# Kernel optimization log

Measured on AMD Instinct MI355X. Metric: run time of the kernel, lower is better.

Reference implementation:

```python
import jax, jax.numpy as jnp
import numpy as np

N = 100_000      # nodes
E = 3_200_000    # edges (avg degree 32)
D_IN = 128
D_H = 128
EPS = 1e-12      # F.normalize eps


def setup_inputs() -> dict:
    key = jax.random.key(0)
    k1, k2, k3 = jax.random.split(key, 3)
    X = jax.random.normal(k1, (N, D_IN), dtype=jnp.float32)
    edge_index = jax.random.randint(k2, (2, E), 0, N, dtype=jnp.int32)
    # GCNConv linear weight (stored as [in, out] for X @ W) and bias
    W = jax.random.normal(k3, (D_IN, D_H), dtype=jnp.float32) / np.sqrt(D_IN)
    b = jnp.zeros((D_H,), dtype=jnp.float32)
    # MessageNorm learnable scale, init 1.0
    scale = jnp.ones((1,), dtype=jnp.float32)
    return {"X": X, "edge_index": edge_index, "W": W, "b": b, "scale": scale}


def reference(X, edge_index, W, b, scale):
    n = X.shape[0]
    loop = jnp.arange(n, dtype=edge_index.dtype)
    src = jnp.concatenate([edge_index[0], loop])  # add self loops
    tgt = jnp.concatenate([edge_index[1], loop])
    # symmetric GCN normalization: D^{-1/2} (A+I) D^{-1/2}
    deg = jax.ops.segment_sum(jnp.ones_like(src, X.dtype), tgt, num_segments=n)
    dinv = jnp.where(deg > 0, jax.lax.rsqrt(deg), 0.0)
    norm = dinv[src] * dinv[tgt]  # [E+N]
    XW = X @ W  # [N, D_H]
    msg = jax.ops.segment_sum(norm[:, None] * XW[src], tgt, num_segments=n) + b
    # MessageNorm(learn_scale=True): l2-normalize msg, rescale by ||x||_2 * scale
    msg_n = msg / jnp.maximum(jnp.linalg.norm(msg, axis=-1, keepdims=True), EPS)
    x_norm = jnp.linalg.norm(X, axis=-1, keepdims=True)
    return jax.nn.gelu(msg_n * x_norm * scale, approximate=False)
```

## Files before the change

kernel.cpp:

```cpp
#include <hip/hip_runtime.h>
#include <math.h>

#define D 128
#define NB 391
#define BSH 8
#define BMASK 255
#define CAP 10240
#define EPB 4096
#define LDA 136

typedef unsigned short ushort_t;
typedef unsigned int uint_t;
typedef __attribute__((ext_vector_type(8))) short bfrag;
typedef __attribute__((ext_vector_type(4))) float ffrag;

__device__ inline ushort_t f2bf(float f) {
    uint_t u = __float_as_uint(f);
    uint_t r = (u + 0x7FFFu + ((u >> 16) & 1u)) >> 16;
    return (ushort_t)r;
}

__global__ __launch_bounds__(256) void k_bin(const int* __restrict__ src,
                                             const int* __restrict__ tgt, int e,
                                             int* __restrict__ bucket_cur,
                                             uint_t* __restrict__ binned,
                                             const float* __restrict__ W,
                                             ushort_t* __restrict__ Wt) {
    __shared__ int lcnt[NB];
    __shared__ int lbase[NB];
    int tid = threadIdx.x;

    if (blockIdx.x < 16) {
        int nrow = blockIdx.x * 8 + (tid >> 5);
        int k0 = (tid & 31) * 4;
        ushort4 o;
        o.x = f2bf(W[(size_t)(k0 + 0) * D + nrow]);
        o.y = f2bf(W[(size_t)(k0 + 1) * D + nrow]);
        o.z = f2bf(W[(size_t)(k0 + 2) * D + nrow]);
        o.w = f2bf(W[(size_t)(k0 + 3) * D + nrow]);
        *(ushort4*)&Wt[(size_t)nrow * D + k0] = o;
    }

    int base = blockIdx.x * EPB;
    for (int i = tid; i < NB; i += 256) lcnt[i] = 0;
    __syncthreads();

    int myb[16], myrank[16];
    uint_t myval[16];
#pragma unroll
    for (int k = 0; k < 16; ++k) {
        int i = base + k * 256 + tid;
        if (i < e) {
            int t = tgt[i];
            int s = src[i];
            int b = t >> BSH;
            myb[k] = b;
            myval[k] = ((uint_t)s << BSH) | (uint_t)(t & BMASK);
            myrank[k] = atomicAdd(&lcnt[b], 1);
        } else {
            myb[k] = -1;
        }
    }
    __syncthreads();
    for (int i = tid; i < NB; i += 256) {
        int c = lcnt[i];
        lbase[i] = (c > 0) ? atomicAdd(&bucket_cur[i], c) : 0;
    }
    __syncthreads();
#pragma unroll
    for (int k = 0; k < 16; ++k) {
        if (myb[k] >= 0) {
            int slot = lbase[myb[k]] + myrank[k];
            if (slot < CAP) binned[(size_t)myb[k] * CAP + slot] = myval[k];
        }
    }
}

__global__ __launch_bounds__(256) void k_sort(const uint_t* __restrict__ binned,
                                              const int* __restrict__ bucket_cur,
                                              int* __restrict__ col,
                                              int* __restrict__ rowptr,
                                              float* __restrict__ dinv, int n) {
    __shared__ uint_t sout[CAP];
    __shared__ int scnt[256];
    __shared__ int sincl[256];
    __shared__ int sofs[256];
    __shared__ int sred[256];
    int b = blockIdx.x;
    int tid = threadIdx.x;

    int v = 0;
    for (int i = tid; i < b; i += 256) v += min(bucket_cur[i], CAP);
    sred[tid] = v;
    __syncthreads();
    for (int off = 128; off >= 1; off >>= 1) {
        if (tid < off) sred[tid] += sred[tid + off];
        __syncthreads();
    }
    int baseg = sred[0];

    int nb = min(bucket_cur[b], CAP);
    const uint_t* bin = binned + (size_t)b * CAP;

    scnt[tid] = 0;
    __syncthreads();
    for (int i = tid; i < nb; i += 256)
        atomicAdd(&scnt[bin[i] & BMASK], 1);
    __syncthreads();
    int x = scnt[tid];
    sincl[tid] = x;
    __syncthreads();
    for (int off = 1; off < 256; off <<= 1) {
        int y = (tid >= off) ? sincl[tid - off] : 0;
        __syncthreads();
        x += y;
        sincl[tid] = x;
        __syncthreads();
    }
    sofs[tid] = x - scnt[tid];
    int t = (b << BSH) + tid;
    if (t < n) {
        rowptr[t + 1] = baseg + x;
        dinv[t] = rsqrtf((float)scnt[tid] + 1.0f);
    }
    if (b == 0 && tid == 0) rowptr[0] = 0;
    __syncthreads();
    for (int i = tid; i < nb; i += 256) {
        uint_t w = bin[i];
        int r = atomicAdd(&sofs[w & BMASK], 1);
        sout[r] = w >> BSH;
    }
    __syncthreads();
    for (int i = tid; i < nb; i += 256)
        col[baseg + i] = (int)sout[i];
}

__global__ __launch_bounds__(256) void k_gemm(const float* __restrict__ X,
                                              const ushort_t* __restrict__ Wt,
                                              const float* __restrict__ dinv,
                                              ushort_t* __restrict__ Y,
                                              float* __restrict__ xnorm, int n) {
    __shared__ ushort_t As[64 * LDA];
    __shared__ ushort_t Bs[128 * LDA];
    int tid = threadIdx.x;
    int row0 = blockIdx.x * 64;

    for (int i = tid; i < 128 * 16; i += 256) {
        int nr = i >> 4, c = (i & 15) << 3;
        *(uint4*)&Bs[nr * LDA + c] = *(const uint4*)&Wt[(size_t)nr * D + c];
    }

    const float4* X4 = (const float4*)X;
#pragma unroll
    for (int i2 = 0; i2 < 8; ++i2) {
        int item = i2 * 256 + tid;
        int r = item >> 5, c4 = item & 31;
        int gr = row0 + r;
        float4 v = (gr < n) ? X4[(size_t)gr * 32 + c4] : make_float4(0.f, 0.f, 0.f, 0.f);
        ushort4 bv;
        bv.x = f2bf(v.x); bv.y = f2bf(v.y); bv.z = f2bf(v.z); bv.w = f2bf(v.w);
        *(ushort4*)&As[r * LDA + c4 * 4] = bv;
        float s = v.x * v.x + v.y * v.y + v.z * v.z + v.w * v.w;
        s += __shfl_xor(s, 1);
        s += __shfl_xor(s, 2);
        s += __shfl_xor(s, 4);
        s += __shfl_xor(s, 8);
        s += __shfl_xor(s, 16);
        if ((tid & 31) == 0 && gr < n) xnorm[gr] = sqrtf(s);
    }
    __syncthreads();

    int w = tid >> 6;
    int lane = tid & 63;
    int q = lane >> 4;
    int mi = lane & 15;

    bfrag xf[4];
#pragma unroll
    for (int kt = 0; kt < 4; ++kt)
        xf[kt] = *(const bfrag*)&As[(w * 16 + mi) * LDA + kt * 32 + q * 8];

    ffrag acc[8];
#pragma unroll
    for (int nt = 0; nt < 8; ++nt) acc[nt] = (ffrag){0.f, 0.f, 0.f, 0.f};

#pragma unroll
    for (int nt = 0; nt < 8; ++nt) {
#pragma unroll
        for (int kt = 0; kt < 4; ++kt) {
            bfrag wf = *(const bfrag*)&Bs[(nt * 16 + mi) * LDA + kt * 32 + q * 8];
            acc[nt] = __builtin_amdgcn_mfma_f32_16x16x32_bf16(wf, xf[kt], acc[nt], 0, 0, 0);
        }
    }

    int gr = row0 + w * 16 + mi;
    if (gr < n) {
        float dv = dinv[gr];
#pragma unroll
        for (int nt = 0; nt < 8; ++nt) {
            ushort4 o;
            o.x = f2bf(acc[nt][0] * dv);
            o.y = f2bf(acc[nt][1] * dv);
            o.z = f2bf(acc[nt][2] * dv);
            o.w = f2bf(acc[nt][3] * dv);
            *(ushort4*)&Y[(size_t)gr * D + nt * 16 + q * 4] = o;
        }
    }
}

__global__ __launch_bounds__(256) void k_agg(const ushort_t* __restrict__ Y,
                                             const float* __restrict__ xnorm,
                                             const float* __restrict__ dinv,
                                             const int* __restrict__ rowptr,
                                             const int* __restrict__ col,
                                             const float* __restrict__ bias,
                                             const float* __restrict__ scale,
                                             float* __restrict__ out, int n) {
    int t = (blockIdx.x * 256 + threadIdx.x) >> 6;
    int lane = threadIdx.x & 63;
    if (t >= n) return;

    const char* Yb = (const char*)Y;
    uint_t lo4 = (uint_t)lane * 4;

    uint_t p = *(const uint_t*)(Yb + (((uint_t)t << 8) + lo4));
    float a0 = __uint_as_float(p << 16);
    float a1 = __uint_as_float(p & 0xFFFF0000u);

    int beg = rowptr[t];
    int end = rowptr[t + 1];
    for (int base = beg; base < end; base += 64) {
        int m = min(end - base, 64);
        uint_t cv = (uint_t)col[base + min(lane, m - 1)];
        int k = 0;
        for (; k + 16 <= m; k += 16) {
            uint_t qv[16];
#pragma unroll
            for (int j = 0; j < 16; ++j) {
                uint_t s = (uint_t)__builtin_amdgcn_readlane((int)cv, k + j);
                qv[j] = *(const uint_t*)(Yb + ((size_t)s << 8) + lo4);
            }
#pragma unroll
            for (int j = 0; j < 16; ++j) {
                a0 += __uint_as_float(qv[j] << 16);
                a1 += __uint_as_float(qv[j] & 0xFFFF0000u);
            }
        }
        for (; k + 4 <= m; k += 4) {
            uint_t qv[4];
#pragma unroll
            for (int j = 0; j < 4; ++j) {
                uint_t s = (uint_t)__builtin_amdgcn_readlane((int)cv, k + j);
                qv[j] = *(const uint_t*)(Yb + ((size_t)s << 8) + lo4);
            }
#pragma unroll
            for (int j = 0; j < 4; ++j) {
                a0 += __uint_as_float(qv[j] << 16);
                a1 += __uint_as_float(qv[j] & 0xFFFF0000u);
            }
        }
        for (; k < m; ++k) {
            uint_t s = (uint_t)__builtin_amdgcn_readlane((int)cv, k);
            uint_t q = *(const uint_t*)(Yb + ((size_t)s << 8) + lo4);
            a0 += __uint_as_float(q << 16);
            a1 += __uint_as_float(q & 0xFFFF0000u);
        }
    }

    float dt = dinv[t];
    float m0 = fmaf(dt, a0, bias[lane * 2]);
    float m1 = fmaf(dt, a1, bias[lane * 2 + 1]);

    float m2 = m0 * m0 + m1 * m1;
#pragma unroll
    for (int m = 32; m >= 1; m >>= 1) m2 += __shfl_xor(m2, m);

    float denom = fmaxf(sqrtf(m2), 1e-12f);
    float fac = xnorm[t] * scale[0] / denom;
    float g0 = m0 * fac;
    float g1 = m1 * fac;
    float2 o;
    o.x = 0.5f * g0 * (1.0f + erff(g0 * 0.70710678118654752440f));
    o.y = 0.5f * g1 * (1.0f + erff(g1 * 0.70710678118654752440f));
    *(float2*)&out[(size_t)t * D + lane * 2] = o;
}


extern "C" void kernel_launch(void* const* d_in, const int* in_sizes, int n_in,
                              void* d_out, int out_size, void* d_ws, size_t ws_size,
                              hipStream_t stream) {
    const float* X     = (const float*)d_in[0];
    const int*   ei    = (const int*)d_in[1];
    const float* W     = (const float*)d_in[2];
    const float* bias  = (const float*)d_in[3];
    const float* scale = (const float*)d_in[4];
    float* out = (float*)d_out;

    int n = in_sizes[0] / D;
    int e = in_sizes[1] / 2;
    const int* src = ei;
    const int* tgt = ei + e;

    char* ws = (char*)d_ws;
    ushort_t* Y = (ushort_t*)ws;   ws += (size_t)n * D * sizeof(ushort_t);
    uint_t* binned = (uint_t*)Y;
    float* dinv = (float*)ws;      ws += (size_t)n * sizeof(float);
    float* xnorm = (float*)ws;     ws += (size_t)n * sizeof(float);
    int* rowptr = (int*)ws;        ws += (size_t)(n + 1) * sizeof(int);
    int* bucket_cur = (int*)ws;    ws += NB * sizeof(int);
    int* col = (int*)ws;           ws += (size_t)e * sizeof(int);
    ushort_t* Wt = (ushort_t*)ws;

    hipMemsetAsync(bucket_cur, 0, NB * sizeof(int), stream);
    k_bin<<<(e + EPB - 1) / EPB, 256, 0, stream>>>(src, tgt, e, bucket_cur, binned, W, Wt);
    k_sort<<<NB, 256, 0, stream>>>(binned, bucket_cur, col, rowptr, dinv, n);
    k_gemm<<<(n + 63) / 64, 256, 0, stream>>>(X, Wt, dinv, Y, xnorm, n);
    k_agg<<<(n + 3) / 4, 256, 0, stream>>>(Y, xnorm, dinv, rowptr, col, bias, scale, out, n);
}
```

Baseline: 308.0 us.

## Fuse per-bucket CSR sort into aggregation kernel and drop separate sort pass

Removes the k_sort kernel. Edges are binned into smaller 64-target buckets, and each aggregation block sorts its own bucket's sources in shared memory before gathering, so the col/rowptr arrays are never written to or read back from global memory. Degrees are now counted with a global atomic per edge in k_bin, and the GEMM computes dinv inline from them. The cost is 3.2M global atomics on deg, and bins get a separate workspace region instead of aliasing Y. There is also overflow risk: CAP=2432 per 64-node bucket, while the expected load is about 2048.

```diff
diff --git a/kernel.cpp b/kernel.cpp
--- a/kernel.cpp
+++ b/kernel.cpp
@@ -2,11 +2,12 @@
 #include <math.h>
 
 #define D 128
-#define NB 391
-#define BSH 8
-#define BMASK 255
-#define CAP 10240
-#define EPB 4096
+#define BSH 6
+#define BMASK 63
+#define NT 64
+#define NB 1563
+#define CAP 2432
+#define EPB 8192
 #define LDA 136
 
 typedef unsigned short ushort_t;
@@ -20,17 +21,18 @@
     return (ushort_t)r;
 }
 
-__global__ __launch_bounds__(256) void k_bin(const int* __restrict__ src,
+__global__ __launch_bounds__(512) void k_bin(const int* __restrict__ src,
                                              const int* __restrict__ tgt, int e,
                                              int* __restrict__ bucket_cur,
                                              uint_t* __restrict__ binned,
+                                             int* __restrict__ deg,
                                              const float* __restrict__ W,
                                              ushort_t* __restrict__ Wt) {
     __shared__ int lcnt[NB];
     __shared__ int lbase[NB];
     int tid = threadIdx.x;
 
-    if (blockIdx.x < 16) {
+    if (blockIdx.x < 16 && tid < 256) {
         int nrow = blockIdx.x * 8 + (tid >> 5);
         int k0 = (tid & 31) * 4;
         ushort4 o;
@@ -42,14 +44,14 @@
     }
 
     int base = blockIdx.x * EPB;
-    for (int i = tid; i < NB; i += 256) lcnt[i] = 0;
+    for (int i = tid; i < NB; i += 512) lcnt[i] = 0;
     __syncthreads();
 
     int myb[16], myrank[16];
     uint_t myval[16];
 #pragma unroll
     for (int k = 0; k < 16; ++k) {
-        int i = base + k * 256 + tid;
+        int i = base + k * 512 + tid;
         if (i < e) {
             int t = tgt[i];
             int s = src[i];
@@ -57,12 +59,13 @@
             myb[k] = b;
             myval[k] = ((uint_t)s << BSH) | (uint_t)(t & BMASK);
             myrank[k] = atomicAdd(&lcnt[b], 1);
+            atomicAdd(&deg[t], 1);
         } else {
             myb[k] = -1;
         }
     }
     __syncthreads();
-    for (int i = tid; i < NB; i += 256) {
+    for (int i = tid; i < NB; i += 512) {
         int c = lcnt[i];
         lbase[i] = (c > 0) ? atomicAdd(&bucket_cur[i], c) : 0;
     }
@@ -76,68 +79,9 @@
     }
 }
 
-__global__ __launch_bounds__(256) void k_sort(const uint_t* __restrict__ binned,
-                                              const int* __restrict__ bucket_cur,
-                                              int* __restrict__ col,
-                                              int* __restrict__ rowptr,
-                                              float* __restrict__ dinv, int n) {
-    __shared__ uint_t sout[CAP];
-    __shared__ int scnt[256];
-    __shared__ int sincl[256];
-    __shared__ int sofs[256];
-    __shared__ int sred[256];
-    int b = blockIdx.x;
-    int tid = threadIdx.x;
-
-    int v = 0;
-    for (int i = tid; i < b; i += 256) v += min(bucket_cur[i], CAP);
-    sred[tid] = v;
-    __syncthreads();
-    for (int off = 128; off >= 1; off >>= 1) {
-        if (tid < off) sred[tid] += sred[tid + off];
-        __syncthreads();
-    }
-    int baseg = sred[0];
-
-    int nb = min(bucket_cur[b], CAP);
-    const uint_t* bin = binned + (size_t)b * CAP;
-
-    scnt[tid] = 0;
-    __syncthreads();
-    for (int i = tid; i < nb; i += 256)
-        atomicAdd(&scnt[bin[i] & BMASK], 1);
-    __syncthreads();
-    int x = scnt[tid];
-    sincl[tid] = x;
-    __syncthreads();
-    for (int off = 1; off < 256; off <<= 1) {
-        int y = (tid >= off) ? sincl[tid - off] : 0;
-        __syncthreads();
-        x += y;
-        sincl[tid] = x;
-        __syncthreads();
-    }
-    sofs[tid] = x - scnt[tid];
-    int t = (b << BSH) + tid;
-    if (t < n) {
-        rowptr[t + 1] = baseg + x;
-        dinv[t] = rsqrtf((float)scnt[tid] + 1.0f);
-    }
-    if (b == 0 && tid == 0) rowptr[0] = 0;
-    __syncthreads();
-    for (int i = tid; i < nb; i += 256) {
-        uint_t w = bin[i];
-        int r = atomicAdd(&sofs[w & BMASK], 1);
-        sout[r] = w >> BSH;
-    }
-    __syncthreads();
-    for (int i = tid; i < nb; i += 256)
-        col[baseg + i] = (int)sout[i];
-}
-
 __global__ __launch_bounds__(256) void k_gemm(const float* __restrict__ X,
                                               const ushort_t* __restrict__ Wt,
-                                              const float* __restrict__ dinv,
+                                              const int* __restrict__ deg,
                                               ushort_t* __restrict__ Y,
                                               float* __restrict__ xnorm, int n) {
     __shared__ ushort_t As[64 * LDA];
@@ -195,7 +139,7 @@
 
     int gr = row0 + w * 16 + mi;
     if (gr < n) {
-        float dv = dinv[gr];
+        float dv = rsqrtf((float)deg[gr] + 1.0f);
 #pragma unroll
         for (int nt = 0; nt < 8; ++nt) {
             ushort4 o;
@@ -210,79 +154,119 @@
 
 __global__ __launch_bounds__(256) void k_agg(const ushort_t* __restrict__ Y,
                                              const float* __restrict__ xnorm,
-                                             const float* __restrict__ dinv,
-                                             const int* __restrict__ rowptr,
-                                             const int* __restrict__ col,
+                                             const uint_t* __restrict__ binned,
+                                             const int* __restrict__ bucket_cur,
                                              const float* __restrict__ bias,
                                              const float* __restrict__ scale,
                                              float* __restrict__ out, int n) {
-    int t = (blockIdx.x * 256 + threadIdx.x) >> 6;
-    int lane = threadIdx.x & 63;
-    if (t >= n) return;
+    __shared__ uint_t ssrc[CAP];
+    __shared__ int scnt[NT];
+    __shared__ int sbeg[NT];
+    __shared__ int sofs[NT];
+    int b = blockIdx.x;
+    int tid = threadIdx.x;
+    int wv = tid >> 6;
+    int lane = tid & 63;
+
+    int nb = min(bucket_cur[b], CAP);
+    const uint_t* bin = binned + (size_t)b * CAP;
+
+    if (tid < NT) scnt[tid] = 0;
+    __syncthreads();
+    for (int i = tid; i < nb; i += 256)
+        atomicAdd(&scnt[bin[i] & BMASK], 1);
+    __syncthreads();
+    if (tid < 64) {
+        int c = scnt[tid];
+        int x = c;
+#pragma unroll
+        for (int off = 1; off < 64; off <<= 1) {
+            int y = __shfl_up(x, off);
+            if (lane >= off) x += y;
+        }
+        sbeg[tid] = x - c;
+        sofs[tid] = x - c;
+    }
+    __syncthreads();
+    for (int i = tid; i < nb; i += 256) {
+        uint_t w = bin[i];
+        int r = atomicAdd(&sofs[w & BMASK], 1);
+        ssrc[r] = w >> BSH;
+    }
+    __syncthreads();
 
     const char* Yb = (const char*)Y;
     uint_t lo4 = (uint_t)lane * 4;
-
-    uint_t p = *(const uint_t*)(Yb + (((uint_t)t << 8) + lo4));
-    float a0 = __uint_as_float(p << 16);
-    float a1 = __uint_as_float(p & 0xFFFF0000u);
-
-    int beg = rowptr[t];
-    int end = rowptr[t + 1];
-    for (int base = beg; base < end; base += 64) {
-        int m = min(end - base, 64);
-        uint_t cv = (uint_t)col[base + min(lane, m - 1)];
-        int k = 0;
-        for (; k + 16 <= m; k += 16) {
-            uint_t qv[16];
-#pragma unroll
-            for (int j = 0; j < 16; ++j) {
-                uint_t s = (uint_t)__builtin_amdgcn_readlane((int)cv, k + j);
-                qv[j] = *(const uint_t*)(Yb + ((size_t)s << 8) + lo4);
+    float b0 = bias[lane * 2];
+    float b1 = bias[lane * 2 + 1];
+    float sc = scale[0];
+
+    for (int i = 0; i < 16; ++i) {
+        int tl = wv * 16 + i;
+        int t = (b << BSH) + tl;
+        if (t >= n) break;
+        int cnt = scnt[tl];
+        int beg = sbeg[tl];
+
+        uint_t p = *(const uint_t*)(Yb + (((uint_t)t << 8) + lo4));
+        float a0 = __uint_as_float(p << 16);
+        float a1 = __uint_as_float(p & 0xFFFF0000u);
+
+        for (int base = 0; base < cnt; base += 64) {
+            int m = min(cnt - base, 64);
+            uint_t cv = ssrc[beg + base + min(lane, m - 1)];
+            int k = 0;
+            for (; k + 16 <= m; k += 16) {
+                uint_t qv[16];
+#pragma unroll
+                for (int j = 0; j < 16; ++j) {
+                    uint_t s = (uint_t)__builtin_amdgcn_readlane((int)cv, k + j);
+                    qv[j] = *(const uint_t*)(Yb + ((size_t)s << 8) + lo4);
+                }
+#pragma unroll
+                for (int j = 0; j < 16; ++j) {
+                    a0 += __uint_as_float(qv[j] << 16);
+                    a1 += __uint_as_float(qv[j] & 0xFFFF0000u);
+                }
             }
-#pragma unroll
-            for (int j = 0; j < 16; ++j) {
-                a0 += __uint_as_float(qv[j] << 16);
-                a1 += __uint_as_float(qv[j] & 0xFFFF0000u);
+            for (; k + 4 <= m; k += 4) {
+                uint_t qv[4];
+#pragma unroll
+                for (int j = 0; j < 4; ++j) {
+                    uint_t s = (uint_t)__builtin_amdgcn_readlane((int)cv, k + j);
+                    qv[j] = *(const uint_t*)(Yb + ((size_t)s << 8) + lo4);
+                }
+#pragma unroll
+                for (int j = 0; j < 4; ++j) {
+                    a0 += __uint_as_float(qv[j] << 16);
+                    a1 += __uint_as_float(qv[j] & 0xFFFF0000u);
+                }
             }
-        }
-        for (; k + 4 <= m; k += 4) {
-            uint_t qv[4];
-#pragma unroll
-            for (int j = 0; j < 4; ++j) {
-                uint_t s = (uint_t)__builtin_amdgcn_readlane((int)cv, k + j);
-                qv[j] = *(const uint_t*)(Yb + ((size_t)s << 8) + lo4);
+            for (; k < m; ++k) {
+                uint_t s = (uint_t)__builtin_amdgcn_readlane((int)cv, k);
+                uint_t q = *(const uint_t*)(Yb + ((size_t)s << 8) + lo4);
+                a0 += __uint_as_float(q << 16);
+                a1 += __uint_as_float(q & 0xFFFF0000u);
             }
-#pragma unroll
-            for (int j = 0; j < 4; ++j) {
-                a0 += __uint_as_float(qv[j] << 16);
-                a1 += __uint_as_float(qv[j] & 0xFFFF0000u);
-            }
-        }
-        for (; k < m; ++k) {
-            uint_t s = (uint_t)__builtin_amdgcn_readlane((int)cv, k);
-            uint_t q = *(const uint_t*)(Yb + ((size_t)s << 8) + lo4);
-            a0 += __uint_as_float(q << 16);
-            a1 += __uint_as_float(q & 0xFFFF0000u);
-        }
-    }
-
-    float dt = dinv[t];
-    float m0 = fmaf(dt, a0, bias[lane * 2]);
-    float m1 = fmaf(dt, a1, bias[lane * 2 + 1]);
-
-    float m2 = m0 * m0 + m1 * m1;
-#pragma unroll
-    for (int m = 32; m >= 1; m >>= 1) m2 += __shfl_xor(m2, m);
-
-    float denom = fmaxf(sqrtf(m2), 1e-12f);
-    float fac = xnorm[t] * scale[0] / denom;
-    float g0 = m0 * fac;
-    float g1 = m1 * fac;
-    float2 o;
-    o.x = 0.5f * g0 * (1.0f + erff(g0 * 0.70710678118654752440f));
-    o.y = 0.5f * g1 * (1.0f + erff(g1 * 0.70710678118654752440f));
-    *(float2*)&out[(size_t)t * D + lane * 2] = o;
+        }
+
+        float dt = rsqrtf((float)cnt + 1.0f);
+        float m0 = fmaf(dt, a0, b0);
+        float m1 = fmaf(dt, a1, b1);
+
+        float m2 = m0 * m0 + m1 * m1;
+#pragma unroll
+        for (int mm = 32; mm >= 1; mm >>= 1) m2 += __shfl_xor(m2, mm);
+
+        float denom = fmaxf(sqrtf(m2), 1e-12f);
+        float fac = xnorm[t] * sc / denom;
+        float g0 = m0 * fac;
+        float g1 = m1 * fac;
+        float2 o;
+        o.x = 0.5f * g0 * (1.0f + erff(g0 * 0.70710678118654752440f));
+        o.y = 0.5f * g1 * (1.0f + erff(g1 * 0.70710678118654752440f));
+        *(float2*)&out[(size_t)t * D + lane * 2] = o;
+    }
 }
 
 
@@ -303,17 +287,14 @@
 
     char* ws = (char*)d_ws;
     ushort_t* Y = (ushort_t*)ws;   ws += (size_t)n * D * sizeof(ushort_t);
-    uint_t* binned = (uint_t*)Y;
-    float* dinv = (float*)ws;      ws += (size_t)n * sizeof(float);
+    uint_t* binned = (uint_t*)ws;  ws += (size_t)NB * CAP * sizeof(uint_t);
     float* xnorm = (float*)ws;     ws += (size_t)n * sizeof(float);
-    int* rowptr = (int*)ws;        ws += (size_t)(n + 1) * sizeof(int);
+    int* deg = (int*)ws;           ws += (size_t)n * sizeof(int);
     int* bucket_cur = (int*)ws;    ws += NB * sizeof(int);
-    int* col = (int*)ws;           ws += (size_t)e * sizeof(int);
     ushort_t* Wt = (ushort_t*)ws;
 
-    hipMemsetAsync(bucket_cur, 0, NB * sizeof(int), stream);
-    k_bin<<<(e + EPB - 1) / EPB, 256, 0, stream>>>(src, tgt, e, bucket_cur, binned, W, Wt);
-    k_sort<<<NB, 256, 0, stream>>>(binned, bucket_cur, col, rowptr, dinv, n);
-    k_gemm<<<(n + 63) / 64, 256, 0, stream>>>(X, Wt, dinv, Y, xnorm, n);
-    k_agg<<<(n + 3) / 4, 256, 0, stream>>>(Y, xnorm, dinv, rowptr, col, bias, scale, out, n);
-}
+    hipMemsetAsync(deg, 0, ((size_t)n + NB) * sizeof(int), stream);
+    k_bin<<<(e + EPB - 1) / EPB, 512, 0, stream>>>(src, tgt, e, bucket_cur, binned, deg, W, Wt);
+    k_gemm<<<(n + 63) / 64, 256, 0, stream>>>(X, Wt, deg, Y, xnorm, n);
+    k_agg<<<NB, 256, 0, stream>>>(Y, xnorm, binned, bucket_cur, bias, scale, out, n);
+}
```

After: 406.7 us. 32.0% more time.

## Stage binned edges and GEMM output in LDS for coalesced global writes

Applied to the files above, without the earlier changes.

The binning kernel now counts per bucket, computes a block-local prefix scan, and scatters edges into shared memory grouped by bucket. It then writes them to the global bins in contiguous runs instead of one scattered 4-byte store per edge. The GEMM epilogue likewise stages the bf16 output tile in LDS and writes full 16-byte row segments to Y. This adds shared memory use, extra barriers and a second LDS atomic pass in exchange for better-coalesced global stores.

```diff
diff --git a/kernel.cpp b/kernel.cpp
--- a/kernel.cpp
+++ b/kernel.cpp
@@ -26,8 +26,12 @@
                                              uint_t* __restrict__ binned,
                                              const float* __restrict__ W,
                                              ushort_t* __restrict__ Wt) {
+    __shared__ uint_t sval[EPB];
+    __shared__ ushort_t sbkt[EPB];
     __shared__ int lcnt[NB];
-    __shared__ int lbase[NB];
+    __shared__ int lbeg[NB];
+    __shared__ int gbase[NB];
+    __shared__ int pscan[256];
     int tid = threadIdx.x;
 
     if (blockIdx.x < 16) {
@@ -45,7 +49,7 @@
     for (int i = tid; i < NB; i += 256) lcnt[i] = 0;
     __syncthreads();
 
-    int myb[16], myrank[16];
+    int myb[16];
     uint_t myval[16];
 #pragma unroll
     for (int k = 0; k < 16; ++k) {
@@ -53,26 +57,54 @@
         if (i < e) {
             int t = tgt[i];
             int s = src[i];
-            int b = t >> BSH;
-            myb[k] = b;
+            myb[k] = t >> BSH;
             myval[k] = ((uint_t)s << BSH) | (uint_t)(t & BMASK);
-            myrank[k] = atomicAdd(&lcnt[b], 1);
+            atomicAdd(&lcnt[myb[k]], 1);
         } else {
             myb[k] = -1;
         }
     }
     __syncthreads();
+
+    int c0 = (2 * tid < NB) ? lcnt[2 * tid] : 0;
+    int c1 = (2 * tid + 1 < NB) ? lcnt[2 * tid + 1] : 0;
+    int x = c0 + c1;
+    pscan[tid] = x;
+    __syncthreads();
+    for (int off = 1; off < 256; off <<= 1) {
+        int y = (tid >= off) ? pscan[tid - off] : 0;
+        __syncthreads();
+        x += y;
+        pscan[tid] = x;
+        __syncthreads();
+    }
+    int pb = x - (c0 + c1);
+    if (2 * tid < NB) lbeg[2 * tid] = pb;
+    if (2 * tid + 1 < NB) lbeg[2 * tid + 1] = pb + c0;
+    __syncthreads();
+
     for (int i = tid; i < NB; i += 256) {
         int c = lcnt[i];
-        lbase[i] = (c > 0) ? atomicAdd(&bucket_cur[i], c) : 0;
-    }
-    __syncthreads();
+        gbase[i] = (c > 0) ? atomicAdd(&bucket_cur[i], c) : 0;
+        lcnt[i] = lbeg[i];
+    }
+    __syncthreads();
+
 #pragma unroll
     for (int k = 0; k < 16; ++k) {
         if (myb[k] >= 0) {
-            int slot = lbase[myb[k]] + myrank[k];
-            if (slot < CAP) binned[(size_t)myb[k] * CAP + slot] = myval[k];
-        }
+            int r = atomicAdd(&lcnt[myb[k]], 1);
+            sval[r] = myval[k];
+            sbkt[r] = (ushort_t)myb[k];
+        }
+    }
+    __syncthreads();
+
+    int nb = min(e - base, EPB);
+    for (int i = tid; i < nb; i += 256) {
+        int b = sbkt[i];
+        int slot = gbase[b] + (i - lbeg[b]);
+        if (slot < CAP) binned[(size_t)b * CAP + slot] = sval[i];
     }
 }
 
@@ -193,17 +225,27 @@
         }
     }
 
+    __syncthreads();
     int gr = row0 + w * 16 + mi;
-    if (gr < n) {
-        float dv = dinv[gr];
-#pragma unroll
-        for (int nt = 0; nt < 8; ++nt) {
-            ushort4 o;
-            o.x = f2bf(acc[nt][0] * dv);
-            o.y = f2bf(acc[nt][1] * dv);
-            o.z = f2bf(acc[nt][2] * dv);
-            o.w = f2bf(acc[nt][3] * dv);
-            *(ushort4*)&Y[(size_t)gr * D + nt * 16 + q * 4] = o;
+    float dv = (gr < n) ? dinv[gr] : 0.f;
+#pragma unroll
+    for (int nt = 0; nt < 8; ++nt) {
+        ushort4 o;
+        o.x = f2bf(acc[nt][0] * dv);
+        o.y = f2bf(acc[nt][1] * dv);
+        o.z = f2bf(acc[nt][2] * dv);
+        o.w = f2bf(acc[nt][3] * dv);
+        *(ushort4*)&As[(w * 16 + mi) * LDA + nt * 16 + q * 4] = o;
+    }
+    __syncthreads();
+
+    int row = tid >> 2, seg = tid & 3;
+    int grow = row0 + row;
+    if (grow < n) {
+#pragma unroll
+        for (int k2 = 0; k2 < 4; ++k2) {
+            uint4 vv = *(const uint4*)&As[row * LDA + seg * 32 + k2 * 8];
+            *(uint4*)&Y[(size_t)grow * D + seg * 32 + k2 * 8] = vv;
         }
     }
 }
```

Result: no change. 305.9 us (-0.7%).
